# Optimization experiments

Hardware: AMD Instinct MI355X
Metric: run time of the kernel (lower is better)

## Reference

```python
import jax, jax.numpy as jnp
import numpy as np

EPS = 1e-12  # matches torch F.normalize default eps


def setup_inputs() -> dict:
    key = jax.random.key(0)
    ks = jax.random.split(key, 8)
    B, N, D, H = 8, 2048, 128, 128
    s = 1.0 / np.sqrt(D)
    return {
        "x": jax.random.normal(ks[0], (B, N, D), dtype=jnp.float32),
        "edge_weight": jax.random.uniform(ks[1], (B, N, N), dtype=jnp.float32),
        "W0": jax.random.normal(ks[2], (D, H), dtype=jnp.float32) * s,
        "b0": jnp.zeros((H,), dtype=jnp.float32),
        "W1": jax.random.normal(ks[3], (H, H), dtype=jnp.float32) * s,
        "b1": jnp.zeros((H,), dtype=jnp.float32),
        "W2": jax.random.normal(ks[4], (H, H), dtype=jnp.float32) * s,
        "b2": jnp.zeros((H,), dtype=jnp.float32),
    }


def _adapt_conv(h, edge_weight, W, b, is_last):
    h = h @ W + b                                   # [B,N,H]
    norm = jnp.linalg.norm(h, axis=-1, keepdims=True)
    nh = h / jnp.maximum(norm, EPS)                 # L2 normalize (F.normalize)
    cos = jnp.einsum('bij,bkj->bik', nh, nh)        # [B,N,N] cosine similarity
    ew = edge_weight * cos                          # elementwise mask
    h = jnp.einsum('bpq,bqc->bpc', ew, h)           # weighted aggregation
    if not is_last:
        h = jax.nn.relu(h)                          # dropout p=0.0 -> identity
    return h


def reference(x, edge_weight, W0, b0, W1, b1, W2, b2):
    params = [(W0, b0), (W1, b1), (W2, b2)]
    h = x
    n_layers = len(params)
    for i, (W, b) in enumerate(params):
        h = _adapt_conv(h, edge_weight, W, b, is_last=(i == n_layers - 1))
    return h
```

## Files before the change

### kernel.cpp

```cpp
#include <hip/hip_runtime.h>
#include <hip/hip_bf16.h>
#include <math.h>


typedef __attribute__((ext_vector_type(8))) short bf16x8;
typedef __attribute__((ext_vector_type(4))) short bf16x4;
typedef __attribute__((ext_vector_type(4))) float f32x4;

static constexpr int kB = 8, kN = 2048, kH = 128;

static __device__ __forceinline__ ushort bf16bits(float f) {
    __hip_bfloat16 hb = __float2bfloat16(f);
    return *reinterpret_cast<ushort*>(&hb);
}

#define LDS_BARRIER()                                          \
    do {                                                       \
        asm volatile("s_waitcnt lgkmcnt(0)" ::: "memory");     \
        __builtin_amdgcn_s_barrier();                          \
        __builtin_amdgcn_sched_barrier(0);                     \
    } while (0)

__global__ __launch_bounds__(256) void cvt_bf16_kernel(
    const float* __restrict__ src, ushort* __restrict__ dst, int n4)
{
    int i = blockIdx.x * 256 + threadIdx.x;
    if (i >= n4) return;
    float4 v = ((const float4*)src)[i];
    bf16x4 o;
    o[0] = (short)bf16bits(v.x); o[1] = (short)bf16bits(v.y);
    o[2] = (short)bf16bits(v.z); o[3] = (short)bf16bits(v.w);
    ((bf16x4*)dst)[i] = o;
}

__global__ __launch_bounds__(256) void cvt_wT_kernel(
    const float* __restrict__ W0, const float* __restrict__ W1,
    const float* __restrict__ W2, ushort* __restrict__ WT)
{
    const float* W = blockIdx.y == 0 ? W0 : (blockIdx.y == 1 ? W1 : W2);
    int i = blockIdx.x * 256 + threadIdx.x;
    int d = i >> 7, c = i & 127;
    WT[(size_t)blockIdx.y * kH * kH + c * kH + d] = bf16bits(W[d * kH + c]);
}

__global__ __launch_bounds__(256) void linear_tr_kernel(
    const ushort* __restrict__ h16, const ushort* __restrict__ WT,
    const float* __restrict__ bias, ushort* __restrict__ t16,
    ushort* __restrict__ tT16, float* __restrict__ invn)
{
    __shared__ float ssb[64][2];
    __shared__ ushort tr[128 * 72];

    const int tid = threadIdx.x, lane = tid & 63, wid = tid >> 6;
    const int wr = wid >> 1, wc = wid & 1, quad = lane >> 4, l16 = lane & 15;
    const int rowbase = blockIdx.x * 64;
    const int b = rowbase / kN, q0 = rowbase % kN;

    f32x4 acc[2][4];
#pragma unroll
    for (int i = 0; i < 2; ++i)
#pragma unroll
        for (int ct = 0; ct < 4; ++ct) acc[i][ct] = (f32x4){0.f, 0.f, 0.f, 0.f};

#pragma unroll
    for (int k = 0; k < 4; ++k) {
        bf16x8 Af[2], Bf[4];
#pragma unroll
        for (int i = 0; i < 2; ++i)
            Af[i] = *(const bf16x8*)&h16[(size_t)(rowbase + wr * 32 + i * 16 + l16) * kH + k * 32 + quad * 8];
#pragma unroll
        for (int ct = 0; ct < 4; ++ct)
            Bf[ct] = *(const bf16x8*)&WT[(size_t)(wc * 64 + ct * 16 + l16) * kH + k * 32 + quad * 8];
#pragma unroll
        for (int i = 0; i < 2; ++i)
#pragma unroll
            for (int ct = 0; ct < 4; ++ct)
                acc[i][ct] = __builtin_amdgcn_mfma_f32_16x16x32_bf16(Af[i], Bf[ct], acc[i][ct], 0, 0, 0);
    }

    float bsr[4];
#pragma unroll
    for (int ct = 0; ct < 4; ++ct) bsr[ct] = bias[wc * 64 + ct * 16 + l16];

    f32x4 ss[2] = {(f32x4){0,0,0,0}, (f32x4){0,0,0,0}};
#pragma unroll
    for (int i = 0; i < 2; ++i)
#pragma unroll
        for (int ct = 0; ct < 4; ++ct)
#pragma unroll
            for (int r = 0; r < 4; ++r) {
                float v = acc[i][ct][r] + bsr[ct];
                acc[i][ct][r] = v;
                ss[i][r] += v * v;
            }
#pragma unroll
    for (int step = 1; step < 16; step <<= 1)
#pragma unroll
        for (int i = 0; i < 2; ++i)
#pragma unroll
            for (int r = 0; r < 4; ++r) ss[i][r] += __shfl_xor(ss[i][r], step);

    if (l16 == 0)
#pragma unroll
        for (int i = 0; i < 2; ++i)
#pragma unroll
            for (int r = 0; r < 4; ++r)
                ssb[wr * 32 + i * 16 + quad * 4 + r][wc] = ss[i][r];
    __syncthreads();
    if (tid < 64) {
        float s2 = ssb[tid][0] + ssb[tid][1];
        invn[rowbase + tid] = 1.f / fmaxf(sqrtf(s2), 1e-12f);
    }

#pragma unroll
    for (int i = 0; i < 2; ++i)
#pragma unroll
        for (int ct = 0; ct < 4; ++ct)
#pragma unroll
            for (int r = 0; r < 4; ++r) {
                const int pl = wr * 32 + i * 16 + quad * 4 + r;
                const int c = wc * 64 + ct * 16 + l16;
                ushort bits = bf16bits(acc[i][ct][r]);
                t16[(size_t)(rowbase + pl) * kH + c] = bits;
                tr[c * 72 + pl] = bits;
            }
    __syncthreads();

    ushort* tTb = tT16 + (size_t)b * kH * kN;
#pragma unroll
    for (int it = 0; it < 4; ++it) {
        int idx = tid + 256 * it;
        int c = idx >> 3, ch = idx & 7;
        bf16x8 v = *(const bf16x8*)&tr[c * 72 + ch * 8];
        *(bf16x8*)&tTb[(size_t)c * kN + q0 + ch * 8] = v;
    }
}

__global__ __launch_bounds__(1024, 4) void agg_kernel(
    const ushort* __restrict__ t, const ushort* __restrict__ tT,
    const float* __restrict__ invn, const float* __restrict__ ew,
    ushort* __restrict__ hout, float* __restrict__ fout, int last)
{
    __shared__ char TQ[2][64 * 256];
    __shared__ char TT[2][128 * 128];
    __shared__ char Spm[64 * 128];
    __shared__ float invPs[64];

    const int b = blockIdx.x, pbase = blockIdx.y * 64;
    const int tid = threadIdx.x, lane = tid & 63, wid = tid >> 6;
    const int wp = wid >> 2, wq = wid & 3, quad = lane >> 4, l16 = lane & 15;

    const ushort* tb  = t  + (size_t)b * kN * kH;
    const ushort* tTb = tT + (size_t)b * kH * kN;
    const float*  ewb = ew + (size_t)b * kN * kN;
    const float*  invb = invn + b * kN;

    if (tid < 64) invPs[tid] = invb[pbase + tid];

    bf16x8 Af[4];
#pragma unroll
    for (int k = 0; k < 4; ++k)
        Af[k] = *(const bf16x8*)&tb[(size_t)(pbase + wp * 16 + l16) * kH + k * 32 + quad * 8];

    const int sqRow = tid >> 4, sqCh = tid & 15;
    const int stRow = tid >> 3, stCh = tid & 7;
    const int sqOff = sqRow * 256 + ((sqCh * 16) ^ ((sqRow & 7) << 4));
    const int stOff = stRow * 128 + ((stCh * 16) ^ ((stRow & 7) << 4));
    bf16x8 rQ = *(const bf16x8*)&tb[(size_t)sqRow * kH + sqCh * 8];
    bf16x8 rT = *(const bf16x8*)&tTb[(size_t)stRow * kN + stCh * 8];

    const int ewRow = pbase + wp * 16 + quad * 4;
    float ewc[4], invQc;
    {
        const int qc = wq * 16 + l16;
        invQc = invb[qc];
#pragma unroll
        for (int r = 0; r < 4; ++r) ewc[r] = ewb[(size_t)(ewRow + r) * kN + qc];
    }

    LDS_BARRIER();
    float invPr[4];
#pragma unroll
    for (int r = 0; r < 4; ++r) invPr[r] = invPs[wp * 16 + quad * 4 + r];

    const int sRow = wq * 16 + l16;
    const int sSwz = (sRow & 7) << 4;
    const int paRow = wp * 16 + l16;
    const int paSwz = (paRow & 7) << 4;

    f32x4 oacc[2] = {(f32x4){0,0,0,0}, (f32x4){0,0,0,0}};

    for (int qt = 0; qt < kN / 64; ++qt) {
        const int s = qt & 1;

        *(bf16x8*)&TQ[s][sqOff] = rQ;
        *(bf16x8*)&TT[s][stOff] = rT;
        LDS_BARRIER();

        float ewn[4] = {0.f, 0.f, 0.f, 0.f};
        float invQn = 0.f;
        if (qt + 1 < kN / 64) {
            const int qb2 = (qt + 1) * 64;
            rQ = *(const bf16x8*)&tb[(size_t)(qb2 + sqRow) * kH + sqCh * 8];
            rT = *(const bf16x8*)&tTb[(size_t)stRow * kN + qb2 + stCh * 8];
            const int qc = qb2 + wq * 16 + l16;
            invQn = invb[qc];
#pragma unroll
            for (int r = 0; r < 4; ++r) ewn[r] = ewb[(size_t)(ewRow + r) * kN + qc];
        }

        f32x4 da0 = (f32x4){0.f, 0.f, 0.f, 0.f};
        f32x4 da1 = (f32x4){0.f, 0.f, 0.f, 0.f};
#pragma unroll
        for (int k = 0; k < 4; k += 2) {
            bf16x8 Bf0 = *(const bf16x8*)&TQ[s][sRow * 256 + ((k * 64 + quad * 16) ^ sSwz)];
            bf16x8 Bf1 = *(const bf16x8*)&TQ[s][sRow * 256 + (((k + 1) * 64 + quad * 16) ^ sSwz)];
            da0 = __builtin_amdgcn_mfma_f32_16x16x32_bf16(Af[k], Bf0, da0, 0, 0, 0);
            da1 = __builtin_amdgcn_mfma_f32_16x16x32_bf16(Af[k + 1], Bf1, da1, 0, 0, 0);
        }
#pragma unroll
        for (int r = 0; r < 4; ++r) {
            const int prow = wp * 16 + quad * 4 + r;
            const int poff = prow * 128 + (((wq * 16 + l16) * 2) ^ ((prow & 7) << 4));
            *(ushort*)&Spm[poff] = bf16bits((da0[r] + da1[r]) * ewc[r] * invQc);
        }
        LDS_BARRIER();

#pragma unroll
        for (int k = 0; k < 2; ++k) {
            bf16x8 Sa = *(const bf16x8*)&Spm[paRow * 128 + ((k * 64 + quad * 16) ^ paSwz)];
#pragma unroll
            for (int ct = 0; ct < 2; ++ct) {
                const int bRow = wq * 32 + ct * 16 + l16;
                bf16x8 Bb = *(const bf16x8*)&TT[s][bRow * 128 + ((k * 64 + quad * 16) ^ ((bRow & 7) << 4))];
                oacc[ct] = __builtin_amdgcn_mfma_f32_16x16x32_bf16(Sa, Bb, oacc[ct], 0, 0, 0);
            }
        }

#pragma unroll
        for (int r = 0; r < 4; ++r) ewc[r] = ewn[r];
        invQc = invQn;
    }

#pragma unroll
    for (int ct = 0; ct < 2; ++ct)
#pragma unroll
        for (int r = 0; r < 4; ++r) {
            const int p = pbase + wp * 16 + quad * 4 + r;
            const int c = wq * 32 + ct * 16 + l16;
            float v = oacc[ct][r] * invPr[r];
            if (!last) {
                hout[(size_t)b * kN * kH + (size_t)p * kH + c] = bf16bits(fmaxf(v, 0.f));
            } else {
                fout[(size_t)b * kN * kH + (size_t)p * kH + c] = v;
            }
        }
}

extern "C" void kernel_launch(void* const* d_in, const int* in_sizes, int n_in,
                              void* d_out, int out_size, void* d_ws, size_t ws_size,
                              hipStream_t stream) {
    const float* x  = (const float*)d_in[0];
    const float* ew = (const float*)d_in[1];
    const float* W0 = (const float*)d_in[2];
    const float* b0 = (const float*)d_in[3];
    const float* W1 = (const float*)d_in[4];
    const float* b1 = (const float*)d_in[5];
    const float* W2 = (const float*)d_in[6];
    const float* b2 = (const float*)d_in[7];
    const float* bias[3] = {b0, b1, b2};

    const size_t nBNH = (size_t)kB * kN * kH;
    ushort* h16  = (ushort*)d_ws;
    ushort* t16  = h16 + nBNH;
    ushort* tT16 = t16 + nBNH;
    float*  invn = (float*)(tT16 + nBNH);
    ushort* WT   = (ushort*)(invn + (size_t)kB * kN);
    float*  out  = (float*)d_out;

    cvt_bf16_kernel<<<(int)(nBNH / 4 + 255) / 256, 256, 0, stream>>>(x, h16, (int)(nBNH / 4));
    cvt_wT_kernel<<<dim3(64, 3), 256, 0, stream>>>(W0, W1, W2, WT);

    for (int layer = 0; layer < 3; ++layer) {
        linear_tr_kernel<<<kB * kN / 64, 256, 0, stream>>>(
            h16, WT + (size_t)layer * kH * kH, bias[layer], t16, tT16, invn);
        agg_kernel<<<dim3(kB, kN / 64), 1024, 0, stream>>>(
            t16, tT16, invn, ew, h16, out, layer == 2 ? 1 : 0);
    }
}
```

Measured before the change: 324.3 us.

## Halve agg_kernel p-tile to 32 rows with 512-thread blocks

```diff
diff --git a/kernel.cpp b/kernel.cpp
--- a/kernel.cpp
+++ b/kernel.cpp
@@ -136,17 +136,17 @@
     }
 }
 
-__global__ __launch_bounds__(1024, 4) void agg_kernel(
+__global__ __launch_bounds__(512, 4) void agg_kernel(
     const ushort* __restrict__ t, const ushort* __restrict__ tT,
     const float* __restrict__ invn, const float* __restrict__ ew,
     ushort* __restrict__ hout, float* __restrict__ fout, int last)
 {
     __shared__ char TQ[2][64 * 256];
     __shared__ char TT[2][128 * 128];
-    __shared__ char Spm[64 * 128];
-    __shared__ float invPs[64];
-
-    const int b = blockIdx.x, pbase = blockIdx.y * 64;
+    __shared__ char Spm[32 * 128];
+    __shared__ float invPs[32];
+
+    const int b = blockIdx.x, pbase = blockIdx.y * 32;
     const int tid = threadIdx.x, lane = tid & 63, wid = tid >> 6;
     const int wp = wid >> 2, wq = wid & 3, quad = lane >> 4, l16 = lane & 15;
 
@@ -155,7 +155,7 @@
     const float*  ewb = ew + (size_t)b * kN * kN;
     const float*  invb = invn + b * kN;
 
-    if (tid < 64) invPs[tid] = invb[pbase + tid];
+    if (tid < 32) invPs[tid] = invb[pbase + tid];
 
     bf16x8 Af[4];
 #pragma unroll
@@ -164,10 +164,19 @@
 
     const int sqRow = tid >> 4, sqCh = tid & 15;
     const int stRow = tid >> 3, stCh = tid & 7;
-    const int sqOff = sqRow * 256 + ((sqCh * 16) ^ ((sqRow & 7) << 4));
-    const int stOff = stRow * 128 + ((stCh * 16) ^ ((stRow & 7) << 4));
-    bf16x8 rQ = *(const bf16x8*)&tb[(size_t)sqRow * kH + sqCh * 8];
-    bf16x8 rT = *(const bf16x8*)&tTb[(size_t)stRow * kN + stCh * 8];
+    int sqOff[2], stOff[2];
+#pragma unroll
+    for (int j = 0; j < 2; ++j) {
+        const int rq = sqRow + j * 32, rt = stRow + j * 64;
+        sqOff[j] = rq * 256 + ((sqCh * 16) ^ ((rq & 7) << 4));
+        stOff[j] = rt * 128 + ((stCh * 16) ^ ((rt & 7) << 4));
+    }
+    bf16x8 rQ[2], rT[2];
+#pragma unroll
+    for (int j = 0; j < 2; ++j) {
+        rQ[j] = *(const bf16x8*)&tb[(size_t)(sqRow + j * 32) * kH + sqCh * 8];
+        rT[j] = *(const bf16x8*)&tTb[(size_t)(stRow + j * 64) * kN + stCh * 8];
+    }
 
     const int ewRow = pbase + wp * 16 + quad * 4;
     float ewc[4], invQc;
@@ -193,16 +202,22 @@
     for (int qt = 0; qt < kN / 64; ++qt) {
         const int s = qt & 1;
 
-        *(bf16x8*)&TQ[s][sqOff] = rQ;
-        *(bf16x8*)&TT[s][stOff] = rT;
+#pragma unroll
+        for (int j = 0; j < 2; ++j) {
+            *(bf16x8*)&TQ[s][sqOff[j]] = rQ[j];
+            *(bf16x8*)&TT[s][stOff[j]] = rT[j];
+        }
         LDS_BARRIER();
 
         float ewn[4] = {0.f, 0.f, 0.f, 0.f};
         float invQn = 0.f;
         if (qt + 1 < kN / 64) {
             const int qb2 = (qt + 1) * 64;
-            rQ = *(const bf16x8*)&tb[(size_t)(qb2 + sqRow) * kH + sqCh * 8];
-            rT = *(const bf16x8*)&tTb[(size_t)stRow * kN + qb2 + stCh * 8];
+#pragma unroll
+            for (int j = 0; j < 2; ++j) {
+                rQ[j] = *(const bf16x8*)&tb[(size_t)(qb2 + sqRow + j * 32) * kH + sqCh * 8];
+                rT[j] = *(const bf16x8*)&tTb[(size_t)(stRow + j * 64) * kN + qb2 + stCh * 8];
+            }
             const int qc = qb2 + wq * 16 + l16;
             invQn = invb[qc];
 #pragma unroll
@@ -284,7 +299,7 @@
     for (int layer = 0; layer < 3; ++layer) {
         linear_tr_kernel<<<kB * kN / 64, 256, 0, stream>>>(
             h16, WT + (size_t)layer * kH * kH, bias[layer], t16, tT16, invn);
-        agg_kernel<<<dim3(kB, kN / 64), 1024, 0, stream>>>(
+        agg_kernel<<<dim3(kB, kN / 32), 512, 0, stream>>>(
             t16, tT16, invn, ew, h16, out, layer == 2 ? 1 : 0);
     }
 }
```

Result: slower. 344.6 us (+6.2%).
